# Kernel tuning notes

Hardware: AMD Instinct MI355X
Metric: run time of the kernel (lower is better)

## Reference

```python
import jax, jax.numpy as jnp
import numpy as np
import math

E = 8192        # number of hyperedges in the batch
IN_DIM = 256
OUT_DIM = 128


def setup_inputs() -> dict:
    key = jax.random.key(0)
    k1, k2, k3, k4 = jax.random.split(key, 4)
    node_embeddings = jax.random.normal(k1, (E, IN_DIM), dtype=jnp.float32)
    # xavier_uniform-like scale for the projection weights
    lim = 1.414 * math.sqrt(6.0 / (IN_DIM + OUT_DIM))
    query_weight = jax.random.uniform(k2, (IN_DIM, OUT_DIM), minval=-lim, maxval=lim, dtype=jnp.float32)
    key_weight = jax.random.uniform(k3, (IN_DIM, OUT_DIM), minval=-lim, maxval=lim, dtype=jnp.float32)
    # binary hypergraph connectivity mask [E, E]; diagonal forced to 1 so no row is fully masked
    mask = jax.random.randint(k4, (E, E), 0, 2, dtype=jnp.int32)
    mask = mask.at[jnp.arange(E), jnp.arange(E)].set(1)
    return {
        "node_embeddings": node_embeddings,
        "query_weight": query_weight,
        "key_weight": key_weight,
        "attention_mask": mask,
    }


def reference(node_embeddings, query_weight, key_weight, attention_mask):
    # QK projections: [E, in] x [in, out] -> [E, out]
    q = node_embeddings @ query_weight
    k = node_embeddings @ key_weight
    # scaled scores [E, E]
    scores = (q @ k.T) / jnp.sqrt(jnp.asarray(OUT_DIM, dtype=q.dtype))
    # masked_fill(mask == 0, -inf)
    scores = jnp.where(attention_mask == 0, jnp.asarray(-jnp.inf, dtype=scores.dtype), scores)
    probs = jax.nn.softmax(scores, axis=1)
    # output aggregates the KEY projections (as in the original code)
    return probs @ k
```

## Files before the change

### kernel.cpp

```cpp
#include <hip/hip_runtime.h>
#include <stdint.h>

#define E_N 8192
#define SPLIT 8
#define CH 16
#define QBLK 64

typedef unsigned short u16;
typedef unsigned int u32;
typedef unsigned long long u64;
typedef __attribute__((ext_vector_type(4))) float f32x4;
typedef __attribute__((ext_vector_type(8))) short bf16x8;
typedef __attribute__((ext_vector_type(4))) unsigned int u32x4;
typedef __attribute__((ext_vector_type(2))) unsigned int u32x2;

union V16 { u32x4 q; bf16x8 h; u16 u[8]; };

static __device__ __forceinline__ u16 f2bf(float f) {
  union { float f; unsigned u; } c; c.f = f;
  unsigned r = c.u + 0x7FFFu + ((c.u >> 16) & 1u);
  return (u16)(r >> 16);
}

constexpr float QS = 1.4426950408889634f / 11.313708498984761f;

__global__ void k_wt(const float* __restrict__ Wq, const float* __restrict__ Wk,
                     u16* __restrict__ wt) {
  int idx = blockIdx.x * 256 + threadIdx.x;
  int mat = idx >> 15, rem = idx & 32767;
  float v = mat ? Wk[rem] : Wq[rem];
  int d = rem >> 7, c = rem & 127;
  wt[(mat * 128 + c) * 256 + d] = f2bf(v);
}

__launch_bounds__(256)
__global__ void k_proj(const float* __restrict__ X, const u16* __restrict__ wt,
                       u16* __restrict__ qg, u16* __restrict__ kg) {
  __shared__ __align__(16) char Xs[64 * 512];
  const int tid = threadIdx.x;
  const int wid = tid >> 6, lane = tid & 63, g = lane >> 4, l15 = lane & 15;
  const int r0 = blockIdx.x * 64;
#pragma unroll
  for (int i = 0; i < 16; ++i) {
    int s = tid + 256 * i;
    int row = s >> 6, c4 = (s & 63) << 2;
    f32x4 v = *(const f32x4*)(X + (size_t)(r0 + row) * 256 + c4);
    u32x2 pk;
    pk[0] = f2bf(v[0]) | ((unsigned)f2bf(v[1]) << 16);
    pk[1] = f2bf(v[2]) | ((unsigned)f2bf(v[3]) << 16);
    *(u32x2*)(Xs + (((row << 9) + (c4 << 1)) ^ ((row & 7) << 4))) = pk;
  }
  __syncthreads();
  bf16x8 xa[8];
  const int arow = wid * 16 + l15;
#pragma unroll
  for (int ks = 0; ks < 8; ++ks) {
    V16 t; t.q = *(const u32x4*)(Xs + (((arow << 9) + (ks << 6) + (g << 4)) ^ ((l15 & 7) << 4)));
    xa[ks] = t.h;
  }
  const f32x4 zero4 = {0.f, 0.f, 0.f, 0.f};
  f32x4 acc[16];
#pragma unroll
  for (int i = 0; i < 16; ++i) acc[i] = zero4;
#pragma unroll
  for (int ct = 0; ct < 16; ++ct) {
    int mat = ct >> 3, c = ((ct & 7) << 4) + l15;
#pragma unroll
    for (int ks = 0; ks < 8; ++ks) {
      V16 b; b.q = *(const u32x4*)(wt + ((mat * 128 + c) * 256 + (ks << 5) + (g << 3)));
      acc[ct] = __builtin_amdgcn_mfma_f32_16x16x32_bf16(xa[ks], b.h, acc[ct], 0, 0, 0);
    }
  }
#pragma unroll
  for (int ct = 0; ct < 16; ++ct) {
    int mat = ct >> 3, c = ((ct & 7) << 4) + l15;
#pragma unroll
    for (int r = 0; r < 4; ++r) {
      int row = r0 + wid * 16 + 4 * g + r;
      float v = acc[ct][r];
      if (mat == 0) qg[row * 128 + c] = f2bf(v * QS);
      else          kg[row * 128 + c] = f2bf(v);
    }
  }
}

__global__ void k_kt(const u16* __restrict__ kg, u16* __restrict__ ktg) {
  __shared__ __align__(16) u16 Ts[64 * 66];
  const int tid = threadIdx.x;
  const int b = blockIdx.x;
  const int r0 = (b >> 1) * 64, c0 = (b & 1) * 64;
#pragma unroll
  for (int i = 0; i < 2; ++i) {
    int s = tid + 256 * i;
    int row = s >> 3, seg = s & 7;
    u32x4 v = *(const u32x4*)(kg + (size_t)(r0 + row) * 128 + c0 + seg * 8);
    unsigned* dst = (unsigned*)((char*)Ts + row * 132 + seg * 16);
    dst[0] = v[0]; dst[1] = v[1]; dst[2] = v[2]; dst[3] = v[3];
  }
  __syncthreads();
#pragma unroll
  for (int i = 0; i < 2; ++i) {
    int s = tid + 256 * i;
    int oc = s >> 3, seg2 = s & 7;
    u16 t[8];
#pragma unroll
    for (int j = 0; j < 8; ++j) t[j] = Ts[(seg2 * 8 + j) * 66 + oc];
    u32x4 o;
    o[0] = t[0] | ((unsigned)t[1] << 16);
    o[1] = t[2] | ((unsigned)t[3] << 16);
    o[2] = t[4] | ((unsigned)t[5] << 16);
    o[3] = t[6] | ((unsigned)t[7] << 16);
    *(u32x4*)(ktg + (size_t)(c0 + oc) * E_N + r0 + seg2 * 8) = o;
  }
}

#define BARRIER() { asm volatile("s_waitcnt lgkmcnt(0)" ::: "memory"); \
                    __builtin_amdgcn_s_barrier(); }

#define LOADREGS(KV1)                                                           \
  {                                                                             \
    const u16* kp = kgp + (size_t)(KV1) * 128;                                  \
    kr0 = *(const u32x4*)(kp);                                                  \
    kr1 = *(const u32x4*)(kp + 16 * 128);                                       \
    kr2 = *(const u32x4*)(kp + 32 * 128);                                       \
    kr3 = *(const u32x4*)(kp + 48 * 128);                                       \
    const u16* tp = ktp + (KV1);                                                \
    tr0 = *(const u32x4*)(tp);                                                  \
    tr1 = *(const u32x4*)(tp + 32 * E_N);                                       \
    tr2 = *(const u32x4*)(tp + 64 * E_N);                                       \
    tr3 = *(const u32x4*)(tp + 96 * E_N);                                       \
  }

#define WRITELDS(KW, TW)                                                        \
  {                                                                             \
    *(u32x4*)((KW) + kofs)          = kr0;                                      \
    *(u32x4*)((KW) + kofs + 4096)   = kr1;                                      \
    *(u32x4*)((KW) + kofs + 8192)   = kr2;                                      \
    *(u32x4*)((KW) + kofs + 12288)  = kr3;                                      \
    *(u32x4*)((TW) + tofs)          = tr0;                                      \
    *(u32x4*)((TW) + tofs + 4096)   = tr1;                                      \
    *(u32x4*)((TW) + tofs + 8192)   = tr2;                                      \
    *(u32x4*)((TW) + tofs + 12288)  = tr3;                                      \
  }

#define MASKLOAD(SET, KV1)                                                      \
  {                                                                             \
    _Pragma("unroll")                                                           \
    for (int t4 = 0; t4 < 4; ++t4)                                              \
      SET[t4] = *(const u32x4*)(mrow + (KV1) + t4 * 16);                        \
  }

#define FSTEP(SUB, KR, TR, KW, TW, MSET, DOM, DOP, DOW)                         \
  {                                                                             \
    f32x4 S[4];                                                                 \
    _Pragma("unroll")                                                           \
    for (int t = 0; t < 4; ++t) S[t] = zero4;                                   \
    _Pragma("unroll")                                                           \
    for (int t = 0; t < 4; ++t) {                                               \
      int krow = t * 16 + l15;                                                  \
      _Pragma("unroll")                                                         \
      for (int ks = 0; ks < 4; ++ks) {                                          \
        V16 kf; kf.q = *(const u32x4*)((KR) + (((krow << 8) + (ks << 6) + (g << 4)) ^ ((l15 & 7) << 4))); \
        S[t] = __builtin_amdgcn_mfma_f32_16x16x32_bf16(kf.h, qf[ks], S[t], 0, 0, 0); \
      }                                                                         \
    }                                                                           \
    _Pragma("unroll")                                                           \
    for (int t = 0; t < 4; ++t) {                                               \
      float p0 = MSET[t][0] ? __builtin_amdgcn_exp2f(S[t][0]) : 0.f;            \
      float p1 = MSET[t][1] ? __builtin_amdgcn_exp2f(S[t][1]) : 0.f;            \
      float p2 = MSET[t][2] ? __builtin_amdgcn_exp2f(S[t][2]) : 0.f;            \
      float p3 = MSET[t][3] ? __builtin_amdgcn_exp2f(S[t][3]) : 0.f;            \
      lacc += (p0 + p1) + (p2 + p3);                                            \
      u32x2 pk;                                                                 \
      pk[0] = f2bf(p0) | ((u32)f2bf(p1) << 16);                                 \
      pk[1] = f2bf(p2) | ((u32)f2bf(p3) << 16);                                 \
      *(u32x2*)(Pw + ((l15 * 128 + (t * 16 + 4 * g) * 2) ^ ((l15 & 7) << 4))) = pk; \
    }                                                                           \
    if (DOM) {                                                                  \
      MASKLOAD(mqa, kvbase + (((st2 + 2 + qb) & 15) << 6))                      \
      MASKLOAD(mqb, kvbase + (((st2 + 3 + qb) & 15) << 6))                      \
    }                                                                           \
    bf16x8 pa0, pa1;                                                            \
    { V16 t2; t2.q = *(const u32x4*)(Pw + ((l15 * 128 + g * 16) ^ ((l15 & 7) << 4))); pa0 = t2.h; } \
    { V16 t2; t2.q = *(const u32x4*)(Pw + ((l15 * 128 + 64 + g * 16) ^ ((l15 & 7) << 4))); pa1 = t2.h; } \
    _Pragma("unroll")                                                           \
    for (int dt = 0; dt < 8; ++dt) {                                            \
      int krow = dt * 16 + l15;                                                 \
      V16 kf0; kf0.q = *(const u32x4*)((TR) + (((krow << 7) + (g << 4)) ^ ((l15 & 7) << 4))); \
      Oacc[dt] = __builtin_amdgcn_mfma_f32_16x16x32_bf16(pa0, kf0.h, Oacc[dt], 0, 0, 0); \
      V16 kf1; kf1.q = *(const u32x4*)((TR) + (((krow << 7) + 64 + (g << 4)) ^ ((l15 & 7) << 4))); \
      Oacc[dt] = __builtin_amdgcn_mfma_f32_16x16x32_bf16(pa1, kf1.h, Oacc[dt], 0, 0, 0); \
    }                                                                           \
    if (DOW) WRITELDS(KW, TW)                                                   \
    if (DOP) {                                                                  \
      const int kvt = kvbase + (((st2 + (SUB) + 2 + qb) & 15) << 6);            \
      LOADREGS(kvt)                                                             \
    }                                                                           \
    if (DOW) BARRIER()                                                          \
  }

__launch_bounds__(256, 2)
__global__ void k_flash(const u16* __restrict__ qg, const u16* __restrict__ kg,
                        const u16* __restrict__ ktg, const int* __restrict__ M,
                        float* __restrict__ Op, float* __restrict__ lp) {
  __shared__ __align__(16) char K0[64 * 256], K1[64 * 256];
  __shared__ __align__(16) char T0[128 * 128], T1[128 * 128];
  __shared__ __align__(16) char Psh[4 * 2048];
  const int tid = threadIdx.x;
  const int wid = tid >> 6, lane = tid & 63, g = lane >> 4, l15 = lane & 15;
  const int bid = blockIdx.x;
  const int split = bid & 7, qb = bid >> 3;
  const int qb0 = qb * QBLK;
  const int kvbase = split * (E_N / SPLIT);
  char* Pw = Psh + wid * 2048;
  const u32* mrow = (const u32*)M + (size_t)(qb0 + wid * 16 + l15) * E_N + 4 * g;
  u32x4 mqa[4], mqb[4];

  const int kr_r = tid >> 4, kr_s = tid & 15;
  const int tr_d = tid >> 3, tr_s = tid & 7;
  const int kofs = ((kr_r << 8) + (kr_s << 4)) ^ ((kr_r & 7) << 4);
  const int tofs = ((tr_d << 7) + (tr_s << 4)) ^ ((tr_d & 7) << 4);
  const u16* kgp = kg + (size_t)kr_r * 128 + kr_s * 8;
  const u16* ktp = ktg + (size_t)tr_d * E_N + tr_s * 8;
  u32x4 kr0, kr1, kr2, kr3, tr0, tr1, tr2, tr3;

  bf16x8 qf[4];
  {
    const u16* qrow = qg + (size_t)(qb0 + wid * 16 + l15) * 128;
#pragma unroll
    for (int ks = 0; ks < 4; ++ks) {
      V16 t; t.q = *(const u32x4*)(qrow + (ks << 5) + (g << 3));
      qf[ks] = t.h;
    }
  }
  const f32x4 zero4 = {0.f, 0.f, 0.f, 0.f};
  f32x4 Oacc[8];
#pragma unroll
  for (int i = 0; i < 8; ++i) Oacc[i] = zero4;
  float lacc = 0.f;

  {
    const int c0 = (qb & 15) << 6;
    const int c1 = ((qb + 1) & 15) << 6;
    MASKLOAD(mqa, kvbase + c0)
    MASKLOAD(mqb, kvbase + c1)
    LOADREGS(kvbase + c0)
    WRITELDS(K0, T0)
    LOADREGS(kvbase + c1)
    BARRIER()
  }

  for (int st2 = 0; st2 < CH; st2 += 2) {
    FSTEP(0, K0, T0, K1, T1, mqa, false, (st2 < 14), true)
    FSTEP(1, K1, T1, K0, T0, mqb, (st2 < 14), (st2 < 14), (st2 < 14))
  }

  {
    float v = lacc;
    v += __shfl_xor(v, 16);
    v += __shfl_xor(v, 32);
    if (lane < 16)
      lp[split * E_N + qb0 + wid * 16 + lane] = v;
  }
  float* op = Op + ((size_t)split * E_N + qb0 + wid * 16) * 128;
#pragma unroll
  for (int dt = 0; dt < 8; ++dt)
#pragma unroll
    for (int r = 0; r < 4; ++r)
      op[(4 * g + r) * 128 + dt * 16 + l15] = Oacc[dt][r];
}

__global__ void k_comb(const float* __restrict__ Op, const float* __restrict__ lp,
                       float* __restrict__ out) {
  int idx4 = blockIdx.x * 256 + threadIdx.x;
  int base = idx4 << 2;
  int e = base >> 7;
  f32x4 o = {0.f, 0.f, 0.f, 0.f};
  float l = 0.f;
#pragma unroll
  for (int s = 0; s < SPLIT; ++s) {
    o += *(const f32x4*)(Op + (size_t)s * (E_N * 128) + base);
    l += lp[s * E_N + e];
  }
  float rl = 1.0f / l;
  o[0] *= rl; o[1] *= rl; o[2] *= rl; o[3] *= rl;
  *(f32x4*)(out + base) = o;
}

extern "C" void kernel_launch(void* const* d_in, const int* in_sizes, int n_in,
                              void* d_out, int out_size, void* d_ws, size_t ws_size,
                              hipStream_t stream) {
  const float* X  = (const float*)d_in[0];
  const float* Wq = (const float*)d_in[1];
  const float* Wk = (const float*)d_in[2];
  const int*   M  = (const int*)d_in[3];
  char* ws = (char*)d_ws;
  u16*   qg   = (u16*)(ws);
  u16*   kg   = (u16*)(ws + (size_t)(2u << 20));
  u16*   ktg  = (u16*)(ws + (size_t)(4u << 20));
  u16*   wt   = (u16*)(ws + (size_t)(6u << 20));
  float* lp   = (float*)(ws + (size_t)(6u << 20) + (128u << 10));
  float* Op   = (float*)(ws + (size_t)(6u << 20) + (512u << 10) + (8u << 20));
  float* out = (float*)d_out;

  k_wt  <<<256, 256, 0, stream>>>(Wq, Wk, wt);
  k_proj<<<128, 256, 0, stream>>>(X, wt, qg, kg);
  k_kt  <<<256, 256, 0, stream>>>(kg, ktg);
  k_flash<<<SPLIT * (E_N / QBLK), 256, 0, stream>>>(qg, kg, ktg, M, Op, lp);
  k_comb<<<(E_N * 128 / 4) / 256, 256, 0, stream>>>(Op, lp, out);
}
```

Before: 122.4 us.

## Single-buffer K/V tiles in LDS and compress mask into bitmask register

Replaces the double-buffered K and K^T shared-memory tiles with a single buffer. The tile is written between two barriers each step instead of ping-ponging. Mask loads are cut from two 16-register sets to one set, which is compressed into a 16-bit bitmask after use. The goal is lower LDS and VGPR use so more blocks or waves fit per CU, at the cost of an extra barrier per step and less overlap between the LDS write and compute.

```diff
diff --git a/kernel.cpp b/kernel.cpp
--- a/kernel.cpp
+++ b/kernel.cpp
@@ -143,68 +143,29 @@
     *(u32x4*)((TW) + tofs + 12288)  = tr3;                                      \
   }
 
-#define MASKLOAD(SET, KV1)                                                      \
+#define MASKLOAD(KV1)                                                           \
   {                                                                             \
     _Pragma("unroll")                                                           \
     for (int t4 = 0; t4 < 4; ++t4)                                              \
-      SET[t4] = *(const u32x4*)(mrow + (KV1) + t4 * 16);                        \
-  }
-
-#define FSTEP(SUB, KR, TR, KW, TW, MSET, DOM, DOP, DOW)                         \
-  {                                                                             \
-    f32x4 S[4];                                                                 \
-    _Pragma("unroll")                                                           \
-    for (int t = 0; t < 4; ++t) S[t] = zero4;                                   \
+      mqn[t4] = *(const u32x4*)(mrow + (KV1) + t4 * 16);                        \
+  }
+
+#define COMPRESS() ({                                                           \
+    u32 _m = 0;                                                                 \
     _Pragma("unroll")                                                           \
     for (int t = 0; t < 4; ++t) {                                               \
-      int krow = t * 16 + l15;                                                  \
       _Pragma("unroll")                                                         \
-      for (int ks = 0; ks < 4; ++ks) {                                          \
-        V16 kf; kf.q = *(const u32x4*)((KR) + (((krow << 8) + (ks << 6) + (g << 4)) ^ ((l15 & 7) << 4))); \
-        S[t] = __builtin_amdgcn_mfma_f32_16x16x32_bf16(kf.h, qf[ks], S[t], 0, 0, 0); \
-      }                                                                         \
+      for (int c = 0; c < 4; ++c)                                               \
+        _m |= (mqn[t][c] != 0) ? (1u << (4 * t + c)) : 0u;                      \
     }                                                                           \
-    _Pragma("unroll")                                                           \
-    for (int t = 0; t < 4; ++t) {                                               \
-      float p0 = MSET[t][0] ? __builtin_amdgcn_exp2f(S[t][0]) : 0.f;            \
-      float p1 = MSET[t][1] ? __builtin_amdgcn_exp2f(S[t][1]) : 0.f;            \
-      float p2 = MSET[t][2] ? __builtin_amdgcn_exp2f(S[t][2]) : 0.f;            \
-      float p3 = MSET[t][3] ? __builtin_amdgcn_exp2f(S[t][3]) : 0.f;            \
-      lacc += (p0 + p1) + (p2 + p3);                                            \
-      u32x2 pk;                                                                 \
-      pk[0] = f2bf(p0) | ((u32)f2bf(p1) << 16);                                 \
-      pk[1] = f2bf(p2) | ((u32)f2bf(p3) << 16);                                 \
-      *(u32x2*)(Pw + ((l15 * 128 + (t * 16 + 4 * g) * 2) ^ ((l15 & 7) << 4))) = pk; \
-    }                                                                           \
-    if (DOM) {                                                                  \
-      MASKLOAD(mqa, kvbase + (((st2 + 2 + qb) & 15) << 6))                      \
-      MASKLOAD(mqb, kvbase + (((st2 + 3 + qb) & 15) << 6))                      \
-    }                                                                           \
-    bf16x8 pa0, pa1;                                                            \
-    { V16 t2; t2.q = *(const u32x4*)(Pw + ((l15 * 128 + g * 16) ^ ((l15 & 7) << 4))); pa0 = t2.h; } \
-    { V16 t2; t2.q = *(const u32x4*)(Pw + ((l15 * 128 + 64 + g * 16) ^ ((l15 & 7) << 4))); pa1 = t2.h; } \
-    _Pragma("unroll")                                                           \
-    for (int dt = 0; dt < 8; ++dt) {                                            \
-      int krow = dt * 16 + l15;                                                 \
-      V16 kf0; kf0.q = *(const u32x4*)((TR) + (((krow << 7) + (g << 4)) ^ ((l15 & 7) << 4))); \
-      Oacc[dt] = __builtin_amdgcn_mfma_f32_16x16x32_bf16(pa0, kf0.h, Oacc[dt], 0, 0, 0); \
-      V16 kf1; kf1.q = *(const u32x4*)((TR) + (((krow << 7) + 64 + (g << 4)) ^ ((l15 & 7) << 4))); \
-      Oacc[dt] = __builtin_amdgcn_mfma_f32_16x16x32_bf16(pa1, kf1.h, Oacc[dt], 0, 0, 0); \
-    }                                                                           \
-    if (DOW) WRITELDS(KW, TW)                                                   \
-    if (DOP) {                                                                  \
-      const int kvt = kvbase + (((st2 + (SUB) + 2 + qb) & 15) << 6);            \
-      LOADREGS(kvt)                                                             \
-    }                                                                           \
-    if (DOW) BARRIER()                                                          \
-  }
+    _m; })
 
 __launch_bounds__(256, 2)
 __global__ void k_flash(const u16* __restrict__ qg, const u16* __restrict__ kg,
                         const u16* __restrict__ ktg, const int* __restrict__ M,
                         float* __restrict__ Op, float* __restrict__ lp) {
-  __shared__ __align__(16) char K0[64 * 256], K1[64 * 256];
-  __shared__ __align__(16) char T0[128 * 128], T1[128 * 128];
+  __shared__ __align__(16) char K0[64 * 256];
+  __shared__ __align__(16) char T0[128 * 128];
   __shared__ __align__(16) char Psh[4 * 2048];
   const int tid = threadIdx.x;
   const int wid = tid >> 6, lane = tid & 63, g = lane >> 4, l15 = lane & 15;
@@ -214,7 +175,7 @@
   const int kvbase = split * (E_N / SPLIT);
   char* Pw = Psh + wid * 2048;
   const u32* mrow = (const u32*)M + (size_t)(qb0 + wid * 16 + l15) * E_N + 4 * g;
-  u32x4 mqa[4], mqb[4];
+  u32x4 mqn[4];
 
   const int kr_r = tid >> 4, kr_s = tid & 15;
   const int tr_d = tid >> 3, tr_s = tid & 7;
@@ -238,21 +199,67 @@
 #pragma unroll
   for (int i = 0; i < 8; ++i) Oacc[i] = zero4;
   float lacc = 0.f;
+  u32 mbcur, mbnxt;
 
   {
-    const int c0 = (qb & 15) << 6;
-    const int c1 = ((qb + 1) & 15) << 6;
-    MASKLOAD(mqa, kvbase + c0)
-    MASKLOAD(mqb, kvbase + c1)
-    LOADREGS(kvbase + c0)
+    const int c0 = kvbase + ((qb & 15) << 6);
+    MASKLOAD(c0)
+    LOADREGS(c0)
     WRITELDS(K0, T0)
-    LOADREGS(kvbase + c1)
+    mbcur = COMPRESS();
     BARRIER()
   }
 
-  for (int st2 = 0; st2 < CH; st2 += 2) {
-    FSTEP(0, K0, T0, K1, T1, mqa, false, (st2 < 14), true)
-    FSTEP(1, K1, T1, K0, T0, mqb, (st2 < 14), (st2 < 14), (st2 < 14))
+  for (int st = 0; st < CH; ++st) {
+    const bool pf = (st < CH - 1);
+    const int nc = kvbase + (((st + 1 + qb) & 15) << 6);
+    if (pf) MASKLOAD(nc)
+
+    f32x4 S[4];
+#pragma unroll
+    for (int t = 0; t < 4; ++t) S[t] = zero4;
+#pragma unroll
+    for (int t = 0; t < 4; ++t) {
+      int krow = t * 16 + l15;
+#pragma unroll
+      for (int ks = 0; ks < 4; ++ks) {
+        V16 kf; kf.q = *(const u32x4*)(K0 + (((krow << 8) + (ks << 6) + (g << 4)) ^ ((l15 & 7) << 4)));
+        S[t] = __builtin_amdgcn_mfma_f32_16x16x32_bf16(kf.h, qf[ks], S[t], 0, 0, 0);
+      }
+    }
+#pragma unroll
+    for (int t = 0; t < 4; ++t) {
+      float p0 = ((mbcur >> (4 * t + 0)) & 1u) ? __builtin_amdgcn_exp2f(S[t][0]) : 0.f;
+      float p1 = ((mbcur >> (4 * t + 1)) & 1u) ? __builtin_amdgcn_exp2f(S[t][1]) : 0.f;
+      float p2 = ((mbcur >> (4 * t + 2)) & 1u) ? __builtin_amdgcn_exp2f(S[t][2]) : 0.f;
+      float p3 = ((mbcur >> (4 * t + 3)) & 1u) ? __builtin_amdgcn_exp2f(S[t][3]) : 0.f;
+      lacc += (p0 + p1) + (p2 + p3);
+      u32x2 pk;
+      pk[0] = f2bf(p0) | ((u32)f2bf(p1) << 16);
+      pk[1] = f2bf(p2) | ((u32)f2bf(p3) << 16);
+      *(u32x2*)(Pw + ((l15 * 128 + (t * 16 + 4 * g) * 2) ^ ((l15 & 7) << 4))) = pk;
+    }
+    if (pf) LOADREGS(nc)
+
+    bf16x8 pa0, pa1;
+    { V16 t2; t2.q = *(const u32x4*)(Pw + ((l15 * 128 + g * 16) ^ ((l15 & 7) << 4))); pa0 = t2.h; }
+    { V16 t2; t2.q = *(const u32x4*)(Pw + ((l15 * 128 + 64 + g * 16) ^ ((l15 & 7) << 4))); pa1 = t2.h; }
+#pragma unroll
+    for (int dt = 0; dt < 8; ++dt) {
+      int krow = dt * 16 + l15;
+      V16 kf0; kf0.q = *(const u32x4*)(T0 + (((krow << 7) + (g << 4)) ^ ((l15 & 7) << 4)));
+      Oacc[dt] = __builtin_amdgcn_mfma_f32_16x16x32_bf16(pa0, kf0.h, Oacc[dt], 0, 0, 0);
+      V16 kf1; kf1.q = *(const u32x4*)(T0 + (((krow << 7) + 64 + (g << 4)) ^ ((l15 & 7) << 4)));
+      Oacc[dt] = __builtin_amdgcn_mfma_f32_16x16x32_bf16(pa1, kf1.h, Oacc[dt], 0, 0, 0);
+    }
+    if (pf) mbnxt = COMPRESS();
+
+    BARRIER()
+    if (pf) {
+      WRITELDS(K0, T0)
+      mbcur = mbnxt;
+      BARRIER()
+    }
   }
 
   {
```

Measured after the change: 142.3 us. +16.3%, slower.

## Double query block to 128 rows with 512-thread blocks and bitmask-compressed mask

Applied to the files above, without the earlier changes.

Each flash block now handles 128 query rows with 8 waves instead of 64 rows with 4. Every K/K^T tile staged in LDS is therefore reused by twice as many waves, and each thread loads half as much per stage. The attention mask is now loaded only one stage ahead and packed into a 16-bit register bitmask, which frees the VGPRs that held two full mask sets. The trade-offs are a barrier on every step, half as many blocks, and launch bounds of 512 threads at 4 blocks, which may tighten register limits.

```diff
diff --git a/kernel.cpp b/kernel.cpp
--- a/kernel.cpp
+++ b/kernel.cpp
@@ -4,7 +4,7 @@
 #define E_N 8192
 #define SPLIT 8
 #define CH 16
-#define QBLK 64
+#define QBLK 128
 
 typedef unsigned short u16;
 typedef unsigned int u32;
@@ -121,37 +121,40 @@
   {                                                                             \
     const u16* kp = kgp + (size_t)(KV1) * 128;                                  \
     kr0 = *(const u32x4*)(kp);                                                  \
-    kr1 = *(const u32x4*)(kp + 16 * 128);                                       \
-    kr2 = *(const u32x4*)(kp + 32 * 128);                                       \
-    kr3 = *(const u32x4*)(kp + 48 * 128);                                       \
+    kr1 = *(const u32x4*)(kp + 64);                                             \
     const u16* tp = ktp + (KV1);                                                \
     tr0 = *(const u32x4*)(tp);                                                  \
-    tr1 = *(const u32x4*)(tp + 32 * E_N);                                       \
-    tr2 = *(const u32x4*)(tp + 64 * E_N);                                       \
-    tr3 = *(const u32x4*)(tp + 96 * E_N);                                       \
+    tr1 = *(const u32x4*)(tp + 32);                                             \
   }
 
 #define WRITELDS(KW, TW)                                                        \
   {                                                                             \
-    *(u32x4*)((KW) + kofs)          = kr0;                                      \
-    *(u32x4*)((KW) + kofs + 4096)   = kr1;                                      \
-    *(u32x4*)((KW) + kofs + 8192)   = kr2;                                      \
-    *(u32x4*)((KW) + kofs + 12288)  = kr3;                                      \
-    *(u32x4*)((TW) + tofs)          = tr0;                                      \
-    *(u32x4*)((TW) + tofs + 4096)   = tr1;                                      \
-    *(u32x4*)((TW) + tofs + 8192)   = tr2;                                      \
-    *(u32x4*)((TW) + tofs + 12288)  = tr3;                                      \
-  }
-
-#define MASKLOAD(SET, KV1)                                                      \
+    *(u32x4*)((KW) + kofs0) = kr0;                                              \
+    *(u32x4*)((KW) + kofs1) = kr1;                                              \
+    *(u32x4*)((TW) + tofs0) = tr0;                                              \
+    *(u32x4*)((TW) + tofs1) = tr1;                                              \
+  }
+
+#define MASKLOAD(KV1)                                                           \
   {                                                                             \
     _Pragma("unroll")                                                           \
     for (int t4 = 0; t4 < 4; ++t4)                                              \
-      SET[t4] = *(const u32x4*)(mrow + (KV1) + t4 * 16);                        \
-  }
-
-#define FSTEP(SUB, KR, TR, KW, TW, MSET, DOM, DOP, DOW)                         \
+      mq[t4] = *(const u32x4*)(mrow + (KV1) + t4 * 16);                         \
+  }
+
+#define COMPRESS() ({                                                           \
+    u32 _m = 0;                                                                 \
+    _Pragma("unroll")                                                           \
+    for (int t = 0; t < 4; ++t) {                                               \
+      _Pragma("unroll")                                                         \
+      for (int c = 0; c < 4; ++c)                                               \
+        _m |= (mq[t][c] != 0) ? (1u << (4 * t + c)) : 0u;                       \
+    }                                                                           \
+    _m; })
+
+#define FSTEP(ST, KR, TR, KW, TW, DOM, DOW, DOP)                                \
   {                                                                             \
+    if (DOM) MASKLOAD(kvbase + ((((ST) + 1 + qb) & 15) << 6))                   \
     f32x4 S[4];                                                                 \
     _Pragma("unroll")                                                           \
     for (int t = 0; t < 4; ++t) S[t] = zero4;                                   \
@@ -166,19 +169,15 @@
     }                                                                           \
     _Pragma("unroll")                                                           \
     for (int t = 0; t < 4; ++t) {                                               \
-      float p0 = MSET[t][0] ? __builtin_amdgcn_exp2f(S[t][0]) : 0.f;            \
-      float p1 = MSET[t][1] ? __builtin_amdgcn_exp2f(S[t][1]) : 0.f;            \
-      float p2 = MSET[t][2] ? __builtin_amdgcn_exp2f(S[t][2]) : 0.f;            \
-      float p3 = MSET[t][3] ? __builtin_amdgcn_exp2f(S[t][3]) : 0.f;            \
+      float p0 = ((mbcur >> (4 * t + 0)) & 1u) ? __builtin_amdgcn_exp2f(S[t][0]) : 0.f; \
+      float p1 = ((mbcur >> (4 * t + 1)) & 1u) ? __builtin_amdgcn_exp2f(S[t][1]) : 0.f; \
+      float p2 = ((mbcur >> (4 * t + 2)) & 1u) ? __builtin_amdgcn_exp2f(S[t][2]) : 0.f; \
+      float p3 = ((mbcur >> (4 * t + 3)) & 1u) ? __builtin_amdgcn_exp2f(S[t][3]) : 0.f; \
       lacc += (p0 + p1) + (p2 + p3);                                            \
       u32x2 pk;                                                                 \
       pk[0] = f2bf(p0) | ((u32)f2bf(p1) << 16);                                 \
       pk[1] = f2bf(p2) | ((u32)f2bf(p3) << 16);                                 \
       *(u32x2*)(Pw + ((l15 * 128 + (t * 16 + 4 * g) * 2) ^ ((l15 & 7) << 4))) = pk; \
-    }                                                                           \
-    if (DOM) {                                                                  \
-      MASKLOAD(mqa, kvbase + (((st2 + 2 + qb) & 15) << 6))                      \
-      MASKLOAD(mqb, kvbase + (((st2 + 3 + qb) & 15) << 6))                      \
     }                                                                           \
     bf16x8 pa0, pa1;                                                            \
     { V16 t2; t2.q = *(const u32x4*)(Pw + ((l15 * 128 + g * 16) ^ ((l15 & 7) << 4))); pa0 = t2.h; } \
@@ -191,21 +190,19 @@
       V16 kf1; kf1.q = *(const u32x4*)((TR) + (((krow << 7) + 64 + (g << 4)) ^ ((l15 & 7) << 4))); \
       Oacc[dt] = __builtin_amdgcn_mfma_f32_16x16x32_bf16(pa1, kf1.h, Oacc[dt], 0, 0, 0); \
     }                                                                           \
+    if (DOM) mbcur = COMPRESS();                                                \
     if (DOW) WRITELDS(KW, TW)                                                   \
-    if (DOP) {                                                                  \
-      const int kvt = kvbase + (((st2 + (SUB) + 2 + qb) & 15) << 6);            \
-      LOADREGS(kvt)                                                             \
-    }                                                                           \
-    if (DOW) BARRIER()                                                          \
-  }
-
-__launch_bounds__(256, 2)
+    if (DOP) LOADREGS(kvbase + ((((ST) + 2 + qb) & 15) << 6))                   \
+    BARRIER()                                                                   \
+  }
+
+__launch_bounds__(512, 4)
 __global__ void k_flash(const u16* __restrict__ qg, const u16* __restrict__ kg,
                         const u16* __restrict__ ktg, const int* __restrict__ M,
                         float* __restrict__ Op, float* __restrict__ lp) {
   __shared__ __align__(16) char K0[64 * 256], K1[64 * 256];
   __shared__ __align__(16) char T0[128 * 128], T1[128 * 128];
-  __shared__ __align__(16) char Psh[4 * 2048];
+  __shared__ __align__(16) char Psh[8 * 2048];
   const int tid = threadIdx.x;
   const int wid = tid >> 6, lane = tid & 63, g = lane >> 4, l15 = lane & 15;
   const int bid = blockIdx.x;
@@ -214,15 +211,18 @@
   const int kvbase = split * (E_N / SPLIT);
   char* Pw = Psh + wid * 2048;
   const u32* mrow = (const u32*)M + (size_t)(qb0 + wid * 16 + l15) * E_N + 4 * g;
-  u32x4 mqa[4], mqb[4];
-
-  const int kr_r = tid >> 4, kr_s = tid & 15;
-  const int tr_d = tid >> 3, tr_s = tid & 7;
-  const int kofs = ((kr_r << 8) + (kr_s << 4)) ^ ((kr_r & 7) << 4);
-  const int tofs = ((tr_d << 7) + (tr_s << 4)) ^ ((tr_d & 7) << 4);
-  const u16* kgp = kg + (size_t)kr_r * 128 + kr_s * 8;
-  const u16* ktp = ktg + (size_t)tr_d * E_N + tr_s * 8;
-  u32x4 kr0, kr1, kr2, kr3, tr0, tr1, tr2, tr3;
+  u32x4 mq[4];
+  u32 mbcur;
+
+  const int k_row = tid >> 3, k_s = tid & 7;
+  const int t_d = tid >> 2, t_s = tid & 3;
+  const int kofs0 = ((k_row << 8) + (k_s << 4)) ^ ((k_row & 7) << 4);
+  const int kofs1 = ((k_row << 8) + ((k_s + 8) << 4)) ^ ((k_row & 7) << 4);
+  const int tofs0 = ((t_d << 7) + (t_s << 4)) ^ ((t_d & 7) << 4);
+  const int tofs1 = ((t_d << 7) + ((t_s + 4) << 4)) ^ ((t_d & 7) << 4);
+  const u16* kgp = kg + (size_t)k_row * 128 + k_s * 8;
+  const u16* ktp = ktg + (size_t)t_d * E_N + t_s * 8;
+  u32x4 kr0, kr1, tr0, tr1;
 
   bf16x8 qf[4];
   {
@@ -240,19 +240,18 @@
   float lacc = 0.f;
 
   {
-    const int c0 = (qb & 15) << 6;
-    const int c1 = ((qb + 1) & 15) << 6;
-    MASKLOAD(mqa, kvbase + c0)
-    MASKLOAD(mqb, kvbase + c1)
-    LOADREGS(kvbase + c0)
+    const int c0 = kvbase + ((qb & 15) << 6);
+    MASKLOAD(c0)
+    LOADREGS(c0)
     WRITELDS(K0, T0)
-    LOADREGS(kvbase + c1)
+    mbcur = COMPRESS();
+    LOADREGS(kvbase + (((qb + 1) & 15) << 6))
     BARRIER()
   }
 
   for (int st2 = 0; st2 < CH; st2 += 2) {
-    FSTEP(0, K0, T0, K1, T1, mqa, false, (st2 < 14), true)
-    FSTEP(1, K1, T1, K0, T0, mqb, (st2 < 14), (st2 < 14), (st2 < 14))
+    FSTEP(st2,     K0, T0, K1, T1, true,        true,        (st2 < 14))
+    FSTEP(st2 + 1, K1, T1, K0, T0, (st2 < 14),  (st2 < 14),  (st2 < 14))
   }
 
   {
@@ -306,6 +305,6 @@
   k_wt  <<<256, 256, 0, stream>>>(Wq, Wk, wt);
   k_proj<<<128, 256, 0, stream>>>(X, wt, qg, kg);
   k_kt  <<<256, 256, 0, stream>>>(kg, ktg);
-  k_flash<<<SPLIT * (E_N / QBLK), 256, 0, stream>>>(qg, kg, ktg, M, Op, lp);
+  k_flash<<<SPLIT * (E_N / QBLK), 512, 0, stream>>>(qg, kg, ktg, M, Op, lp);
   k_comb<<<(E_N * 128 / 4) / 256, 256, 0, stream>>>(Op, lp, out);
 }
```

Result: slower. 324.4 us (+165.0%).
